# Performance work log

Measured on AMD Instinct MI355X. Metric: run time of the kernel, lower is better.

## Reference

```python
import jax, jax.numpy as jnp
import numpy as np

C_S, C_Z, C_H = 384, 128, 32
N, L = 4, 384
EPS = 1e-5  # torch LayerNorm default


def setup_inputs() -> dict:
    key = jax.random.key(0)
    ks = jax.random.split(key, 8)
    s = jax.random.normal(ks[0], (N, L, C_S), dtype=jnp.float32)
    ln_g = jnp.ones((C_S,), jnp.float32)
    ln_b = jnp.zeros((C_S,), jnp.float32)
    W1 = jax.random.normal(ks[1], (C_S, C_H), jnp.float32) / np.sqrt(C_S)
    b1 = jax.random.normal(ks[2], (C_H,), jnp.float32) * 0.02
    W2 = jax.random.normal(ks[3], (C_S, C_H), jnp.float32) / np.sqrt(C_S)
    b2 = jax.random.normal(ks[4], (C_H,), jnp.float32) * 0.02
    # linear_out has init='final' (zeros) in training; use random values for a
    # meaningful numerical baseline.
    Wo = jax.random.normal(ks[5], (C_H * C_H, C_Z), jnp.float32) / np.sqrt(C_H * C_H)
    bo = jax.random.normal(ks[6], (C_Z,), jnp.float32) * 0.02
    return {"s": s, "ln_g": ln_g, "ln_b": ln_b, "W1": W1, "b1": b1,
            "W2": W2, "b2": b2, "Wo": Wo, "bo": bo}


def reference(s, ln_g, ln_b, W1, b1, W2, b2, Wo, bo):
    # LayerNorm over c_s
    mu = jnp.mean(s, axis=-1, keepdims=True)
    var = jnp.mean(jnp.square(s - mu), axis=-1, keepdims=True)
    sn = (s - mu) * jax.lax.rsqrt(var + EPS) * ln_g + ln_b
    a = sn @ W1 + b1  # [N, L, c_h]
    b = sn @ W2 + b2  # [N, L, c_h]
    # Original: outer product a[n,i,c]*b[n,j,d] flattened as c*c_h+d, then linear_out.
    # Algebraically fused: never materialize the [N,L,L,c_h^2] tensor.
    Wo3 = Wo.reshape(C_H, C_H, C_Z)  # index order (c, d, z) matches c*c_h+d flattening
    z = jnp.einsum('nic,njd,cdz->nijz', a, b, Wo3, optimize=True) + bo
    return z  # [N, L, L, c_z]
```

## Files before the change

### kernel.cpp

```cpp
#include <hip/hip_runtime.h>
#include <hip/hip_bf16.h>

#define CS 384
#define CH 32
#define CZ 128
#define LL 384
#define NL 1536
#define EPS 1e-5f

typedef float v4f __attribute__((ext_vector_type(4)));
typedef short s8v __attribute__((ext_vector_type(8)));
typedef unsigned short u8s __attribute__((ext_vector_type(8)));

static __device__ __forceinline__ unsigned short f2bf(float x) {
    unsigned int b = __float_as_uint(x);
    b += 0x7FFFu + ((b >> 16) & 1u);
    return (unsigned short)(b >> 16);
}
static __device__ __forceinline__ v4f bf4_to_f4(ushort4 h) {
    v4f r;
    r.x = __uint_as_float((unsigned)h.x << 16);
    r.y = __uint_as_float((unsigned)h.y << 16);
    r.z = __uint_as_float((unsigned)h.z << 16);
    r.w = __uint_as_float((unsigned)h.w << 16);
    return r;
}

__global__ __launch_bounds__(256) void k_bf(
    const float* __restrict__ s, const float* __restrict__ g, const float* __restrict__ be,
    const float* __restrict__ W2, const float* __restrict__ pb2,
    const float* __restrict__ Wo,
    unsigned short* __restrict__ BfG, unsigned short* __restrict__ Wob)
{
    const int r0 = blockIdx.x * 4;
    const int t  = threadIdx.x;

    {
        const int idx = blockIdx.x * 256 + t;
        if (idx < (CH * CH * CZ) / 4) {
            const v4f v = ((const v4f*)Wo)[idx];
            ushort4 h;
            h.x = f2bf(v.x); h.y = f2bf(v.y); h.z = f2bf(v.z); h.w = f2bf(v.w);
            ((ushort4*)Wob)[idx] = h;
        }
    }

    __shared__ float sn[4][392];
    __shared__ float part[4][2][32];

    {
        const int w = t >> 6, lane = t & 63;
        const float* srow = s + (size_t)(r0 + w) * CS;
        float x[6];
        #pragma unroll
        for (int k = 0; k < 6; ++k) x[k] = srow[lane + k * 64];
        float p = x[0] + x[1] + x[2] + x[3] + x[4] + x[5];
        #pragma unroll
        for (int m = 1; m < 64; m <<= 1) p += __shfl_xor(p, m);
        const float mu = p * (1.0f / CS);
        float q = 0.f;
        #pragma unroll
        for (int k = 0; k < 6; ++k) { float d = x[k] - mu; q += d * d; }
        #pragma unroll
        for (int m = 1; m < 64; m <<= 1) q += __shfl_xor(q, m);
        const float rstd = rsqrtf(q * (1.0f / CS) + EPS);
        #pragma unroll
        for (int k = 0; k < 6; ++k) {
            const int c = lane + k * 64;
            sn[w][c] = (x[k] - mu) * rstd * g[c] + be[c];
        }
    }
    __syncthreads();

    {
        const int h = t & 31, ch = (t >> 5) & 1, rw = t >> 6;
        const float* snr = sn[rw];
        float acc = 0.f;
        const int c0 = ch * 192;
        #pragma unroll 8
        for (int c = c0; c < c0 + 192; ++c)
            acc += snr[c] * W2[c * CH + h];
        part[rw][ch][h] = acc;
    }
    __syncthreads();

    if (t < 128) {
        const int rw = t >> 5, h = t & 31;
        const float v = part[rw][0][h] + part[rw][1][h] + pb2[h];
        const int row = r0 + rw;
        const int n = row / LL, jr = row % LL;
        const int jt = jr >> 4, l16 = jr & 15;
        BfG[(((size_t)(n * 24 + jt)) * 64 + l16 + 16 * (h >> 3)) * 8 + (h & 7)] = f2bf(v);
    }
}

__global__ __launch_bounds__(256, 3) void k_out_f(
    const float* __restrict__ s, const float* __restrict__ g, const float* __restrict__ be,
    const float* __restrict__ W1, const float* __restrict__ pb1,
    const unsigned short* __restrict__ Wob, const unsigned short* __restrict__ BfG,
    const float* __restrict__ bo, float* __restrict__ out)
{
    const int b  = blockIdx.x;
    const int r0 = b * 2;
    const int n  = r0 / LL;
    const int t  = threadIdx.x;
    const int l = t & 63, w = t >> 6;
    const int g2 = l >> 4, c16 = l & 15;
    const int li = l & 31, hi2 = l >> 5;

    s8v af[6];
    {
        const s8v* Bfn = (const s8v*)(BfG + (size_t)n * 24 * 64 * 8);
        #pragma unroll
        for (int i = 0; i < 6; ++i) af[i] = Bfn[(w + i * 4) * 64 + l];
    }
    v4f bov[8];
    #pragma unroll
    for (int zt = 0; zt < 8; ++zt) bov[zt] = *(const v4f*)(bo + zt * 16 + g2 * 4);

    __shared__ __align__(16) char smem[16384 + 32768];
    unsigned short* MsubT = (unsigned short*)smem;
    float (*sn)[392]      = (float(*)[392])(smem + 16384);
    float (*part)[4][32]  = (float(*)[4][32])(smem + 16384 + 3200);
    float* Afl            = (float*)(smem + 16384 + 3200 + 1024);
    char*  bounceBase     = smem + 16384;

    if (w < 2) {
        const float* srow = s + (size_t)(r0 + w) * CS;
        float x[6];
        #pragma unroll
        for (int k = 0; k < 6; ++k) x[k] = srow[l + k * 64];
        float p = x[0] + x[1] + x[2] + x[3] + x[4] + x[5];
        #pragma unroll
        for (int m = 1; m < 64; m <<= 1) p += __shfl_xor(p, m);
        const float mu = p * (1.0f / CS);
        float q = 0.f;
        #pragma unroll
        for (int k = 0; k < 6; ++k) { float d = x[k] - mu; q += d * d; }
        #pragma unroll
        for (int m = 1; m < 64; m <<= 1) q += __shfl_xor(q, m);
        const float rstd = rsqrtf(q * (1.0f / CS) + EPS);
        #pragma unroll
        for (int k = 0; k < 6; ++k) {
            const int c = l + k * 64;
            sn[w][c] = (x[k] - mu) * rstd * g[c] + be[c];
        }
    }
    __syncthreads();

    {
        const int h = t & 31, cs = (t >> 5) & 3, rw = t >> 7;
        const float* snr = sn[rw];
        float acc = 0.f;
        const int c0 = cs * 96;
        #pragma unroll 8
        for (int c = c0; c < c0 + 96; ++c)
            acc += snr[c] * W1[c * CH + h];
        part[rw][cs][h] = acc;
    }
    __syncthreads();
    if (t < 64) {
        const int rw = t >> 5, h = t & 31;
        Afl[rw * 32 + h] = part[rw][0][h] + part[rw][1][h] + part[rw][2][h]
                         + part[rw][3][h] + pb1[h];
    }
    __syncthreads();

    {
        const ushort4* Wo4 = (const ushort4*)Wob;
        #pragma unroll
        for (int it = 0; it < 4; ++it) {
            const int col = t + it * 256;
            const int d = col >> 5, zq = col & 31;
            v4f a0 = (v4f)(0.f), a1 = (v4f)(0.f);
            #pragma unroll 8
            for (int c = 0; c < CH; ++c) {
                const v4f wv = bf4_to_f4(Wo4[(size_t)c * 1024 + col]);
                a0 += Afl[c] * wv;
                a1 += Afl[32 + c] * wv;
            }
            const int bsw = ((d >> 3) ^ (zq & 3)) * 8 + (d & 7);
            #pragma unroll
            for (int j = 0; j < 4; ++j) {
                const int z = zq * 4 + j;
                MsubT[z * 32 + bsw]        = f2bf(a0[j]);
                MsubT[4096 + z * 32 + bsw] = f2bf(a1[j]);
            }
        }
    }
    __syncthreads();

    char* myl = bounceBase + w * 8192;
    const int rblk = (g2 ^ ((c16 >> 2) & 3)) * 8;

    #pragma unroll
    for (int rr = 0; rr < 2; ++rr) {
        s8v mf[8];
        {
            const unsigned short* Ms = MsubT + rr * 4096;
            #pragma unroll
            for (int zt = 0; zt < 8; ++zt)
                mf[zt] = *(const s8v*)(Ms + (zt * 16 + c16) * 32 + rblk);
        }

        v4f* outv = (v4f*)(out + (size_t)(r0 + rr) * LL * CZ);

        #pragma unroll
        for (int i = 0; i < 6; ++i) {
            const int jt = w + i * 4;

            #pragma unroll
            for (int zt = 0; zt < 8; ++zt) {
                v4f d = __builtin_amdgcn_mfma_f32_16x16x32_bf16(mf[zt], af[i], (v4f)(0.f), 0, 0, 0);
                d += bov[zt];
                const int byte = (c16 << 9) + (((zt << 6) + (g2 << 4)) ^ ((c16 & 7) << 4));
                *(v4f*)(myl + byte) = d;
            }
            asm volatile("s_waitcnt lgkmcnt(0)" ::: "memory");

            #pragma unroll
            for (int i2 = 0; i2 < 8; ++i2) {
                const int rw2 = 2 * i2 + hi2;
                const int byte = (rw2 << 9) + (((li << 4)) ^ ((rw2 & 7) << 4));
                const v4f v = *(const v4f*)(myl + byte);
                outv[(size_t)(jt * 16 + rw2) * 32 + li] = v;
            }
        }
    }
}

extern "C" void kernel_launch(void* const* d_in, const int* in_sizes, int n_in,
                              void* d_out, int out_size, void* d_ws, size_t ws_size,
                              hipStream_t stream) {
    const float* s  = (const float*)d_in[0];
    const float* g  = (const float*)d_in[1];
    const float* be = (const float*)d_in[2];
    const float* W1 = (const float*)d_in[3];
    const float* b1 = (const float*)d_in[4];
    const float* W2 = (const float*)d_in[5];
    const float* b2 = (const float*)d_in[6];
    const float* Wo = (const float*)d_in[7];
    const float* bo = (const float*)d_in[8];
    float* out = (float*)d_out;

    if (ws_size < 98304u + 262144u) return;
    unsigned short* Bf  = (unsigned short*)d_ws;
    unsigned short* Wob = (unsigned short*)((char*)d_ws + 98304);

    k_bf   <<<NL / 4, 256, 0, stream>>>(s, g, be, W2, b2, Wo, Bf, Wob);
    k_out_f<<<NL / 2, 256, 0, stream>>>(s, g, be, W1, b1, Wob, Bf, bo, out);
}
```

Measured before the change: 79.33 us.

## Give each wave one output row and drop block-wide barriers in output kernel

New measurement: 105.3 us. +32.8%, slower.

```diff
diff --git a/kernel.cpp b/kernel.cpp
--- a/kernel.cpp
+++ b/kernel.cpp
@@ -94,39 +94,38 @@
     }
 }
 
-__global__ __launch_bounds__(256, 3) void k_out_f(
+__global__ __launch_bounds__(128) void k_out_f(
     const float* __restrict__ s, const float* __restrict__ g, const float* __restrict__ be,
     const float* __restrict__ W1, const float* __restrict__ pb1,
     const unsigned short* __restrict__ Wob, const unsigned short* __restrict__ BfG,
     const float* __restrict__ bo, float* __restrict__ out)
 {
-    const int b  = blockIdx.x;
-    const int r0 = b * 2;
+    const int r0 = blockIdx.x * 2;
     const int n  = r0 / LL;
     const int t  = threadIdx.x;
-    const int l = t & 63, w = t >> 6;
+    const int l  = t & 63, w = t >> 6;
+    const int r  = r0 + w;
     const int g2 = l >> 4, c16 = l & 15;
     const int li = l & 31, hi2 = l >> 5;
 
-    s8v af[6];
+    __shared__ __align__(16) unsigned short MsubT[2][4096];
+    __shared__ __align__(16) char ovl[2][8192];
+    __shared__ float aW[2][32];
+
+    s8v af[24];
     {
         const s8v* Bfn = (const s8v*)(BfG + (size_t)n * 24 * 64 * 8);
         #pragma unroll
-        for (int i = 0; i < 6; ++i) af[i] = Bfn[(w + i * 4) * 64 + l];
+        for (int i = 0; i < 24; ++i) af[i] = Bfn[i * 64 + l];
     }
     v4f bov[8];
     #pragma unroll
     for (int zt = 0; zt < 8; ++zt) bov[zt] = *(const v4f*)(bo + zt * 16 + g2 * 4);
 
-    __shared__ __align__(16) char smem[16384 + 32768];
-    unsigned short* MsubT = (unsigned short*)smem;
-    float (*sn)[392]      = (float(*)[392])(smem + 16384);
-    float (*part)[4][32]  = (float(*)[4][32])(smem + 16384 + 3200);
-    float* Afl            = (float*)(smem + 16384 + 3200 + 1024);
-    char*  bounceBase     = smem + 16384;
-
-    if (w < 2) {
-        const float* srow = s + (size_t)(r0 + w) * CS;
+    float* sn = (float*)ovl[w];
+
+    {
+        const float* srow = s + (size_t)r * CS;
         float x[6];
         #pragma unroll
         for (int k = 0; k < 6; ++k) x[k] = srow[l + k * 64];
@@ -143,88 +142,72 @@
         #pragma unroll
         for (int k = 0; k < 6; ++k) {
             const int c = l + k * 64;
-            sn[w][c] = (x[k] - mu) * rstd * g[c] + be[c];
-        }
-    }
-    __syncthreads();
-
-    {
-        const int h = t & 31, cs = (t >> 5) & 3, rw = t >> 7;
-        const float* snr = sn[rw];
+            sn[c] = (x[k] - mu) * rstd * g[c] + be[c];
+        }
+    }
+    asm volatile("s_waitcnt lgkmcnt(0)" ::: "memory");
+
+    {
+        const int h = l & 31, half = l >> 5;
         float acc = 0.f;
-        const int c0 = cs * 96;
+        const int c0 = half * 192;
         #pragma unroll 8
-        for (int c = c0; c < c0 + 96; ++c)
-            acc += snr[c] * W1[c * CH + h];
-        part[rw][cs][h] = acc;
-    }
-    __syncthreads();
-    if (t < 64) {
-        const int rw = t >> 5, h = t & 31;
-        Afl[rw * 32 + h] = part[rw][0][h] + part[rw][1][h] + part[rw][2][h]
-                         + part[rw][3][h] + pb1[h];
-    }
-    __syncthreads();
+        for (int c = c0; c < c0 + 192; ++c)
+            acc += sn[c] * W1[c * CH + h];
+        acc += __shfl_xor(acc, 32);
+        if (l < 32) aW[w][l] = acc + pb1[l];
+    }
+    asm volatile("s_waitcnt lgkmcnt(0)" ::: "memory");
+
+    float aw[CH];
+    #pragma unroll
+    for (int c = 0; c < CH; ++c) aw[c] = aW[w][c];
 
     {
         const ushort4* Wo4 = (const ushort4*)Wob;
         #pragma unroll
-        for (int it = 0; it < 4; ++it) {
-            const int col = t + it * 256;
+        for (int it = 0; it < 16; ++it) {
+            const int col = l + it * 64;
             const int d = col >> 5, zq = col & 31;
-            v4f a0 = (v4f)(0.f), a1 = (v4f)(0.f);
+            v4f a0 = (v4f)(0.f);
             #pragma unroll 8
-            for (int c = 0; c < CH; ++c) {
-                const v4f wv = bf4_to_f4(Wo4[(size_t)c * 1024 + col]);
-                a0 += Afl[c] * wv;
-                a1 += Afl[32 + c] * wv;
-            }
+            for (int c = 0; c < CH; ++c)
+                a0 += aw[c] * bf4_to_f4(Wo4[(size_t)c * 1024 + col]);
             const int bsw = ((d >> 3) ^ (zq & 3)) * 8 + (d & 7);
             #pragma unroll
-            for (int j = 0; j < 4; ++j) {
-                const int z = zq * 4 + j;
-                MsubT[z * 32 + bsw]        = f2bf(a0[j]);
-                MsubT[4096 + z * 32 + bsw] = f2bf(a1[j]);
-            }
-        }
-    }
-    __syncthreads();
-
-    char* myl = bounceBase + w * 8192;
-    const int rblk = (g2 ^ ((c16 >> 2) & 3)) * 8;
-
-    #pragma unroll
-    for (int rr = 0; rr < 2; ++rr) {
-        s8v mf[8];
-        {
-            const unsigned short* Ms = MsubT + rr * 4096;
-            #pragma unroll
-            for (int zt = 0; zt < 8; ++zt)
-                mf[zt] = *(const s8v*)(Ms + (zt * 16 + c16) * 32 + rblk);
-        }
-
-        v4f* outv = (v4f*)(out + (size_t)(r0 + rr) * LL * CZ);
-
-        #pragma unroll
-        for (int i = 0; i < 6; ++i) {
-            const int jt = w + i * 4;
-
-            #pragma unroll
-            for (int zt = 0; zt < 8; ++zt) {
-                v4f d = __builtin_amdgcn_mfma_f32_16x16x32_bf16(mf[zt], af[i], (v4f)(0.f), 0, 0, 0);
-                d += bov[zt];
-                const int byte = (c16 << 9) + (((zt << 6) + (g2 << 4)) ^ ((c16 & 7) << 4));
-                *(v4f*)(myl + byte) = d;
-            }
-            asm volatile("s_waitcnt lgkmcnt(0)" ::: "memory");
-
-            #pragma unroll
-            for (int i2 = 0; i2 < 8; ++i2) {
-                const int rw2 = 2 * i2 + hi2;
-                const int byte = (rw2 << 9) + (((li << 4)) ^ ((rw2 & 7) << 4));
-                const v4f v = *(const v4f*)(myl + byte);
-                outv[(size_t)(jt * 16 + rw2) * 32 + li] = v;
-            }
+            for (int j = 0; j < 4; ++j)
+                MsubT[w][(zq * 4 + j) * 32 + bsw] = f2bf(a0[j]);
+        }
+    }
+    asm volatile("s_waitcnt lgkmcnt(0)" ::: "memory");
+
+    s8v mf[8];
+    {
+        const int rblk = (g2 ^ ((c16 >> 2) & 3)) * 8;
+        #pragma unroll
+        for (int zt = 0; zt < 8; ++zt)
+            mf[zt] = *(const s8v*)(&MsubT[w][(zt * 16 + c16) * 32 + rblk]);
+    }
+
+    char* myl = ovl[w];
+    v4f* outv = (v4f*)(out + (size_t)r * LL * CZ);
+
+    for (int jt = 0; jt < 24; ++jt) {
+        #pragma unroll
+        for (int zt = 0; zt < 8; ++zt) {
+            v4f d = __builtin_amdgcn_mfma_f32_16x16x32_bf16(mf[zt], af[jt], (v4f)(0.f), 0, 0, 0);
+            d += bov[zt];
+            const int byte = (c16 << 9) + (((zt << 6) + (g2 << 4)) ^ ((c16 & 7) << 4));
+            *(v4f*)(myl + byte) = d;
+        }
+        asm volatile("s_waitcnt lgkmcnt(0)" ::: "memory");
+
+        #pragma unroll
+        for (int i2 = 0; i2 < 8; ++i2) {
+            const int rw2 = 2 * i2 + hi2;
+            const int byte = (rw2 << 9) + (((li << 4)) ^ ((rw2 & 7) << 4));
+            const v4f v = *(const v4f*)(myl + byte);
+            outv[(size_t)(jt * 16 + rw2) * 32 + li] = v;
         }
     }
 }
@@ -248,5 +231,5 @@
     unsigned short* Wob = (unsigned short*)((char*)d_ws + 98304);
 
     k_bf   <<<NL / 4, 256, 0, stream>>>(s, g, be, W2, b2, Wo, Bf, Wob);
-    k_out_f<<<NL / 2, 256, 0, stream>>>(s, g, be, W1, b1, Wob, Bf, bo, out);
-}
+    k_out_f<<<NL / 2, 128, 0, stream>>>(s, g, be, W1, b1, Wob, Bf, bo, out);
+}
```
